# Kernel tuning notes

Measured on AMD Instinct MI355X. Metric: run time of the kernel, lower is better.

The kernel has to match this reference:

```python
import jax, jax.numpy as jnp
import numpy as np

NEG = -1.0e9

def setup_inputs() -> dict:
    key = jax.random.key(0)
    ks = jax.random.split(key, 4)
    B, S, D, DK = 4, 2048, 1024, 128
    inputs = jax.random.normal(ks[0], (B, S, D), dtype=jnp.float32)
    scale = 1.0 / np.sqrt(D)
    Wq = jax.random.normal(ks[1], (D, DK), dtype=jnp.float32) * scale
    Wk = jax.random.normal(ks[2], (D, DK), dtype=jnp.float32) * scale
    Wv = jax.random.normal(ks[3], (D, DK), dtype=jnp.float32) * scale
    bq = jnp.zeros((DK,), dtype=jnp.float32)
    bk = jnp.zeros((DK,), dtype=jnp.float32)
    bv = jnp.zeros((DK,), dtype=jnp.float32)
    return {"inputs": inputs, "Wq": Wq, "bq": bq, "Wk": Wk, "bk": bk, "Wv": Wv, "bv": bv}

def reference(inputs, Wq, bq, Wk, bk, Wv, bv):
    # Q/K/V projections: Dense(d_k) on last dim
    Q = jnp.einsum('bsd,dk->bsk', inputs, Wq) + bq
    K = jnp.einsum('bsd,dk->bsk', inputs, Wk) + bk
    V = jnp.einsum('bsd,dk->bsk', inputs, Wv) + bv
    d_k = Q.shape[-1]
    S = inputs.shape[1]
    # FAITHFUL to original bug: mask = lower-triangular ones, added *-1e9
    # (masks the lower triangle including the diagonal, NOT the upper).
    mask = jnp.tril(jnp.ones((S, S), dtype=inputs.dtype))
    scores = jnp.einsum('bqk,bsk->bqs', Q, K) / jnp.sqrt(jnp.asarray(d_k, inputs.dtype))
    masked_scores = scores + mask * NEG  # [B, S, S]
    attn = jax.nn.softmax(masked_scores, axis=-1)
    out = jnp.einsum('bqs,bsk->bqk', attn, V)  # [B, S, d_k]
    return out
```

## Files before the change

### kernel.cpp

```cpp
#include <hip/hip_runtime.h>
#include <hip/hip_bf16.h>

typedef __attribute__((ext_vector_type(8))) short bf16x8;
typedef __attribute__((ext_vector_type(4))) float f32x4;

#define QSCALE 0.088388347648318447f

__device__ __forceinline__ unsigned short f2bf(float f) {
  __hip_bfloat16 h = __float2bfloat16(f);
  unsigned short u;
  __builtin_memcpy(&u, &h, 2);
  return u;
}
__device__ __forceinline__ float bf2f(unsigned short u) {
  unsigned int x = ((unsigned int)u) << 16;
  float f; __builtin_memcpy(&f, &x, 4);
  return f;
}

__device__ __forceinline__ void gload_lds16(void* lds, const void* g) {
  __builtin_amdgcn_global_load_lds(
      (const __attribute__((address_space(1))) unsigned int*)g,
      (__attribute__((address_space(3))) unsigned int*)lds, 16, 0, 0);
}

__global__ __launch_bounds__(256) void cvt_x(const float* __restrict__ x,
                                             unsigned short* __restrict__ xb) {
  int i = (blockIdx.x * 256 + threadIdx.x) * 8;
  float4 v0 = *reinterpret_cast<const float4*>(x + i);
  float4 v1 = *reinterpret_cast<const float4*>(x + i + 4);
  ushort4 o0, o1;
  o0.x = f2bf(v0.x); o0.y = f2bf(v0.y); o0.z = f2bf(v0.z); o0.w = f2bf(v0.w);
  o1.x = f2bf(v1.x); o1.y = f2bf(v1.y); o1.z = f2bf(v1.z); o1.w = f2bf(v1.w);
  *reinterpret_cast<ushort4*>(xb + i) = o0;
  *reinterpret_cast<ushort4*>(xb + i + 4) = o1;
}

__global__ __launch_bounds__(256) void cvt_w(const float* __restrict__ Wq,
                                             const float* __restrict__ Wk,
                                             const float* __restrict__ Wv,
                                             unsigned short* __restrict__ Wt) {
  int idx = blockIdx.x * 256 + threadIdx.x;
  int n = idx >> 10, d = idx & 1023;
  const float* W = (n < 128) ? Wq : (n < 256 ? Wk : Wv);
  float v = W[d * 128 + (n & 127)];
  if (n < 128) v *= QSCALE;
  Wt[idx] = f2bf(v);
}

__global__ __launch_bounds__(256) void proj_gemm(
    const unsigned short* __restrict__ Xb, const unsigned short* __restrict__ Wt,
    const float* __restrict__ bq, const float* __restrict__ bk, const float* __restrict__ bv,
    unsigned short* __restrict__ Qb, unsigned short* __restrict__ Kb,
    unsigned short* __restrict__ Vt) {
  __shared__ unsigned short sA[64 * 64];
  __shared__ unsigned short sB[64 * 64];
  const int nt = blockIdx.x % 6;
  const int mt = blockIdx.x / 6;
  const int m0 = mt * 64;
  const int n0 = nt * 64;
  const int tid = threadIdx.x;
  const int lane = tid & 63;
  const int w = tid >> 6;
  const int r = lane & 15, g = lane >> 4;
  const int wm = (w >> 1) * 32, wn = (w & 1) * 32;

  f32x4 acc[2][2];
  #pragma unroll
  for (int mi = 0; mi < 2; ++mi)
    #pragma unroll
    for (int ni = 0; ni < 2; ++ni)
      acc[mi][ni] = (f32x4){0.f, 0.f, 0.f, 0.f};

  const char* Ab = (const char*)Xb;
  const char* Bb = (const char*)Wt;
  char* sAb = (char*)sA;
  char* sBb = (char*)sB;

  for (int k0 = 0; k0 < 1024; k0 += 64) {
    #pragma unroll
    for (int j = 0; j < 2; ++j) {
      int f = j * 4096 + tid * 16;
      int row = f >> 7;
      int colb = f & 127;
      gload_lds16(sAb + f, Ab + ((size_t)(m0 + row) * 1024 + k0) * 2 + colb);
      gload_lds16(sBb + f, Bb + ((size_t)(n0 + row) * 1024 + k0) * 2 + colb);
    }
    __syncthreads();
    #pragma unroll
    for (int kk = 0; kk < 2; ++kk) {
      bf16x8 af[2], bfr[2];
      #pragma unroll
      for (int mi = 0; mi < 2; ++mi)
        af[mi] = *reinterpret_cast<const bf16x8*>(sA + (wm + mi * 16 + r) * 64 + kk * 32 + g * 8);
      #pragma unroll
      for (int ni = 0; ni < 2; ++ni)
        bfr[ni] = *reinterpret_cast<const bf16x8*>(sB + (wn + ni * 16 + r) * 64 + kk * 32 + g * 8);
      #pragma unroll
      for (int mi = 0; mi < 2; ++mi)
        #pragma unroll
        for (int ni = 0; ni < 2; ++ni)
          acc[mi][ni] = __builtin_amdgcn_mfma_f32_16x16x32_bf16(af[mi], bfr[ni], acc[mi][ni], 0, 0, 0);
    }
    __syncthreads();
  }

  const float* bias = (nt < 2) ? bq : (nt < 4 ? bk : bv);
  const float bsc = (nt < 2) ? QSCALE : 1.0f;
  #pragma unroll
  for (int mi = 0; mi < 2; ++mi) {
    #pragma unroll
    for (int ni = 0; ni < 2; ++ni) {
      const int colg = n0 + wn + ni * 16 + r;
      const int colm = colg & 127;
      const float bias_v = bias[colm] * bsc;
      #pragma unroll
      for (int e = 0; e < 4; ++e) {
        const int row = m0 + wm + mi * 16 + g * 4 + e;
        const unsigned short hh = f2bf(acc[mi][ni][e] + bias_v);
        if (nt < 2) Qb[(size_t)row * 128 + colm] = hh;
        else if (nt < 4) Kb[(size_t)row * 128 + colm] = hh;
        else {
          const int bb = row >> 11, s = row & 2047;
          Vt[((size_t)bb * 128 + colm) * 2048 + s] = hh;
        }
      }
    }
  }
}

__global__ __launch_bounds__(512, 4) void attn(
    const unsigned short* __restrict__ Qb, const unsigned short* __restrict__ Kb,
    const unsigned short* __restrict__ Vt,
    float* __restrict__ po, float* __restrict__ pl) {
  __shared__ char sK[2][8192];
  __shared__ char sV[2][8192];
  __shared__ unsigned short pbuf_s[8][512];
  const int tid = threadIdx.x;
  const int lane = tid & 63;
  const int w = tid >> 6;
  const int r = lane & 15, g = lane >> 4;
  const int sig = blockIdx.x & 7;
  const int b = (blockIdx.x >> 3) & 3;
  const int p = blockIdx.x >> 5;

  const char* Kg = (const char*)(Kb + (size_t)b * 2048 * 128);
  const char* Vg = (const char*)(Vt + (size_t)b * 128 * 2048);
  unsigned short* pbuf = pbuf_s[w];

  const int krow = tid >> 4;
  const int kcol = ((tid & 15) * 16) ^ ((krow & 7) * 16);
  const int vrow = tid >> 2;
  const int vcol = ((tid & 3) * 16) ^ ((vrow & 3) * 16);

  for (int phase = 0; phase < 2; ++phase) {
    const int t = phase ? (15 - p) : p;
    const int q0b = t << 7;
    const int ntiles = (2048 - q0b) >> 5;
    const int q0w = q0b + w * 16;

    const unsigned short* Q = Qb + (size_t)(b * 2048 + q0w) * 128;
    bf16x8 qf[4];
    #pragma unroll
    for (int kk = 0; kk < 4; ++kk)
      qf[kk] = *reinterpret_cast<const bf16x8*>(Q + r * 128 + kk * 32 + g * 8);

    f32x4 o[8];
    #pragma unroll
    for (int ni = 0; ni < 8; ++ni) o[ni] = (f32x4){0.f, 0.f, 0.f, 0.f};
    float l[4];
    #pragma unroll
    for (int e = 0; e < 4; ++e) l[e] = 0.f;

    const int nT = (ntiles > sig) ? ((ntiles - sig + 7) >> 3) : 0;

    if (nT > 0) {
      const int s0 = q0b + (sig << 5);
      gload_lds16(&sK[0][tid * 16], Kg + (size_t)(s0 + krow) * 256 + kcol);
      gload_lds16(&sV[0][tid * 16], Vg + (size_t)vrow * 4096 + (size_t)s0 * 2 + vcol);
    }
    for (int it = 0; it < nT; ++it) {
      const int cur = it & 1;
      const int s0 = q0b + ((sig + (it << 3)) << 5);
      if (it + 1 < nT) {
        const int s1 = s0 + 256;
        gload_lds16(&sK[cur ^ 1][tid * 16], Kg + (size_t)(s1 + krow) * 256 + kcol);
        gload_lds16(&sV[cur ^ 1][tid * 16], Vg + (size_t)vrow * 4096 + (size_t)s1 * 2 + vcol);
        asm volatile("s_waitcnt vmcnt(2)" ::: "memory");
      } else {
        asm volatile("s_waitcnt vmcnt(0)" ::: "memory");
      }
      asm volatile("s_barrier" ::: "memory");

      f32x4 st[2];
      #pragma unroll
      for (int sj = 0; sj < 2; ++sj) {
        f32x4 a = (f32x4){0.f, 0.f, 0.f, 0.f};
        #pragma unroll
        for (int kk = 0; kk < 4; ++kk) {
          const bf16x8 kf = *reinterpret_cast<const bf16x8*>(
              &sK[cur][(sj * 16 + r) * 256 + (((kk * 64 + g * 16) ^ ((r & 7) * 16)))]);
          a = __builtin_amdgcn_mfma_f32_16x16x32_bf16(qf[kk], kf, a, 0, 0, 0);
        }
        st[sj] = a;
      }
      #pragma unroll
      for (int sj = 0; sj < 2; ++sj) {
        const int s = s0 + sj * 16 + r;
        #pragma unroll
        for (int e = 0; e < 4; ++e) {
          const int q = q0w + g * 4 + e;
          st[sj][e] = (s <= q) ? 0.f : __expf(st[sj][e]);
        }
      }
      #pragma unroll
      for (int e = 0; e < 4; ++e) l[e] += st[0][e] + st[1][e];

      #pragma unroll
      for (int sj = 0; sj < 2; ++sj)
        #pragma unroll
        for (int e = 0; e < 4; ++e)
          pbuf[(g * 4 + e) * 32 + sj * 16 + r] = f2bf(st[sj][e]);
      asm volatile("s_waitcnt lgkmcnt(0)" ::: "memory");
      __builtin_amdgcn_sched_barrier(0);
      const bf16x8 pa = *reinterpret_cast<const bf16x8*>(&pbuf[r * 32 + g * 8]);

      #pragma unroll
      for (int ni = 0; ni < 8; ++ni) {
        const bf16x8 vf = *reinterpret_cast<const bf16x8*>(
            &sV[cur][(ni * 16 + r) * 64 + ((g * 16) ^ ((r & 3) * 16))]);
        o[ni] = __builtin_amdgcn_mfma_f32_16x16x32_bf16(pa, vf, o[ni], 0, 0, 0);
      }
      asm volatile("s_waitcnt lgkmcnt(0)" ::: "memory");
      __builtin_amdgcn_sched_barrier(0);
      asm volatile("s_barrier" ::: "memory");
    }

    #pragma unroll
    for (int off = 1; off < 16; off <<= 1)
      #pragma unroll
      for (int e = 0; e < 4; ++e)
        l[e] += __shfl_xor(l[e], off, 64);

    const size_t pb = ((size_t)((b * 16 + t) * 8 + sig)) * 16384;
    #pragma unroll
    for (int ni = 0; ni < 8; ++ni)
      #pragma unroll
      for (int e = 0; e < 4; ++e)
        po[pb + (size_t)(w * 16 + g * 4 + e) * 128 + ni * 16 + r] = o[ni][e];
    if (r == 0) {
      #pragma unroll
      for (int e = 0; e < 4; ++e)
        pl[((size_t)((b * 16 + t) * 8 + sig)) * 128 + w * 16 + g * 4 + e] = l[e];
    }
  }
}

__global__ __launch_bounds__(256) void combine(const float* __restrict__ po,
                                               const float* __restrict__ pl,
                                               float* __restrict__ out) {
  const int idx = blockIdx.x * 256 + threadIdx.x;
  const int d = idx & 127;
  const int gq = idx >> 7;
  const int b = gq >> 11, q = gq & 2047;
  const int qt = q >> 7, row = q & 127;
  const size_t base = (size_t)(b * 16 + qt) * 8;
  float o = 0.f, l = 0.f;
  #pragma unroll
  for (int s = 0; s < 8; ++s) {
    o += po[(base + s) * 16384 + row * 128 + d];
    l += pl[(base + s) * 128 + row];
  }
  out[idx] = (l > 0.f) ? o / l : 0.f;
}

__global__ __launch_bounds__(64) void lastrow(const unsigned short* __restrict__ Vt,
                                              float* __restrict__ out) {
  const int b = blockIdx.x >> 7;
  const int dk = blockIdx.x & 127;
  const unsigned short* row = Vt + (size_t)(b * 128 + dk) * 2048;
  float s = 0.f;
  for (int i = threadIdx.x; i < 2048; i += 64) s += bf2f(row[i]);
  #pragma unroll
  for (int off = 32; off > 0; off >>= 1) s += __shfl_down(s, off, 64);
  if (threadIdx.x == 0) out[(size_t)(b * 2048 + 2047) * 128 + dk] = s * (1.0f / 2048.0f);
}

extern "C" void kernel_launch(void* const* d_in, const int* in_sizes, int n_in,
                              void* d_out, int out_size, void* d_ws, size_t ws_size,
                              hipStream_t stream) {
  const float* x  = (const float*)d_in[0];
  const float* Wq = (const float*)d_in[1];
  const float* bq = (const float*)d_in[2];
  const float* Wk = (const float*)d_in[3];
  const float* bk = (const float*)d_in[4];
  const float* Wv = (const float*)d_in[5];
  const float* bv = (const float*)d_in[6];
  float* out = (float*)d_out;
  char* ws = (char*)d_ws;
  unsigned short* Xb = (unsigned short*)(ws);
  unsigned short* Wt = (unsigned short*)(ws + (size_t)(16u << 20));
  unsigned short* Qb = (unsigned short*)(ws + (size_t)(17u << 20));
  unsigned short* Kb = (unsigned short*)(ws + (size_t)(19u << 20));
  unsigned short* Vt = (unsigned short*)(ws + (size_t)(21u << 20));
  float* po = (float*)(ws + (size_t)(24u << 20));
  float* pl = (float*)(ws + (size_t)(56u << 20));

  hipLaunchKernelGGL(cvt_x, dim3(4096), dim3(256), 0, stream, x, Xb);
  hipLaunchKernelGGL(cvt_w, dim3(1536), dim3(256), 0, stream, Wq, Wk, Wv, Wt);
  hipLaunchKernelGGL(proj_gemm, dim3(768), dim3(256), 0, stream,
                     Xb, Wt, bq, bk, bv, Qb, Kb, Vt);
  hipLaunchKernelGGL(attn, dim3(256), dim3(512), 0, stream, Qb, Kb, Vt, po, pl);
  hipLaunchKernelGGL(combine, dim3(4096), dim3(256), 0, stream, po, pl, out);
  hipLaunchKernelGGL(lastrow, dim3(512), dim3(64), 0, stream, Vt, out);
}
```

Baseline: 71.83 us.

## Merge conversion kernels and enlarge projection GEMM tiles to 128x96

Merges the input and weight bf16 conversion kernels into one launch, removing a kernel launch and its gap. Reworks the projection GEMM to use 512-thread blocks computing 128x96 output tiles instead of 64x64, so 256 blocks cover the full 8192x384 output. Bias and destination selection now happen per column because a tile can straddle the Q, K and V boundaries. Larger tiles reuse each loaded operand for more MFMAs, but the grid is only 256 blocks, roughly one per CU, so there is less latency hiding.

```diff
diff --git a/kernel.cpp b/kernel.cpp
--- a/kernel.cpp
+++ b/kernel.cpp
@@ -24,52 +24,54 @@
       (__attribute__((address_space(3))) unsigned int*)lds, 16, 0, 0);
 }
 
-__global__ __launch_bounds__(256) void cvt_x(const float* __restrict__ x,
-                                             unsigned short* __restrict__ xb) {
-  int i = (blockIdx.x * 256 + threadIdx.x) * 8;
-  float4 v0 = *reinterpret_cast<const float4*>(x + i);
-  float4 v1 = *reinterpret_cast<const float4*>(x + i + 4);
-  ushort4 o0, o1;
-  o0.x = f2bf(v0.x); o0.y = f2bf(v0.y); o0.z = f2bf(v0.z); o0.w = f2bf(v0.w);
-  o1.x = f2bf(v1.x); o1.y = f2bf(v1.y); o1.z = f2bf(v1.z); o1.w = f2bf(v1.w);
-  *reinterpret_cast<ushort4*>(xb + i) = o0;
-  *reinterpret_cast<ushort4*>(xb + i + 4) = o1;
-}
-
-__global__ __launch_bounds__(256) void cvt_w(const float* __restrict__ Wq,
-                                             const float* __restrict__ Wk,
-                                             const float* __restrict__ Wv,
-                                             unsigned short* __restrict__ Wt) {
-  int idx = blockIdx.x * 256 + threadIdx.x;
-  int n = idx >> 10, d = idx & 1023;
-  const float* W = (n < 128) ? Wq : (n < 256 ? Wk : Wv);
-  float v = W[d * 128 + (n & 127)];
-  if (n < 128) v *= QSCALE;
-  Wt[idx] = f2bf(v);
-}
-
-__global__ __launch_bounds__(256) void proj_gemm(
+__global__ __launch_bounds__(256) void cvt(const float* __restrict__ x,
+                                           unsigned short* __restrict__ xb,
+                                           const float* __restrict__ Wq,
+                                           const float* __restrict__ Wk,
+                                           const float* __restrict__ Wv,
+                                           unsigned short* __restrict__ Wt) {
+  const int bid = blockIdx.x;
+  if (bid < 4096) {
+    int i = (bid * 256 + threadIdx.x) * 8;
+    float4 v0 = *reinterpret_cast<const float4*>(x + i);
+    float4 v1 = *reinterpret_cast<const float4*>(x + i + 4);
+    ushort4 o0, o1;
+    o0.x = f2bf(v0.x); o0.y = f2bf(v0.y); o0.z = f2bf(v0.z); o0.w = f2bf(v0.w);
+    o1.x = f2bf(v1.x); o1.y = f2bf(v1.y); o1.z = f2bf(v1.z); o1.w = f2bf(v1.w);
+    *reinterpret_cast<ushort4*>(xb + i) = o0;
+    *reinterpret_cast<ushort4*>(xb + i + 4) = o1;
+  } else {
+    int idx = (bid - 4096) * 256 + threadIdx.x;
+    int n = idx >> 10, d = idx & 1023;
+    const float* W = (n < 128) ? Wq : (n < 256 ? Wk : Wv);
+    float v = W[d * 128 + (n & 127)];
+    if (n < 128) v *= QSCALE;
+    Wt[idx] = f2bf(v);
+  }
+}
+
+__global__ __launch_bounds__(512) void proj_gemm(
     const unsigned short* __restrict__ Xb, const unsigned short* __restrict__ Wt,
     const float* __restrict__ bq, const float* __restrict__ bk, const float* __restrict__ bv,
     unsigned short* __restrict__ Qb, unsigned short* __restrict__ Kb,
     unsigned short* __restrict__ Vt) {
-  __shared__ unsigned short sA[64 * 64];
-  __shared__ unsigned short sB[64 * 64];
-  const int nt = blockIdx.x % 6;
-  const int mt = blockIdx.x / 6;
-  const int m0 = mt * 64;
-  const int n0 = nt * 64;
+  __shared__ unsigned short sA[128 * 64];
+  __shared__ unsigned short sB[96 * 64];
+  const int nt = blockIdx.x & 3;
+  const int mt = blockIdx.x >> 2;
+  const int m0 = mt * 128;
+  const int n0 = nt * 96;
   const int tid = threadIdx.x;
   const int lane = tid & 63;
   const int w = tid >> 6;
   const int r = lane & 15, g = lane >> 4;
-  const int wm = (w >> 1) * 32, wn = (w & 1) * 32;
-
-  f32x4 acc[2][2];
+  const int wm = (w >> 1) * 32, wn = (w & 1) * 48;
+
+  f32x4 acc[2][3];
   #pragma unroll
   for (int mi = 0; mi < 2; ++mi)
     #pragma unroll
-    for (int ni = 0; ni < 2; ++ni)
+    for (int ni = 0; ni < 3; ++ni)
       acc[mi][ni] = (f32x4){0.f, 0.f, 0.f, 0.f};
 
   const char* Ab = (const char*)Xb;
@@ -80,46 +82,54 @@
   for (int k0 = 0; k0 < 1024; k0 += 64) {
     #pragma unroll
     for (int j = 0; j < 2; ++j) {
-      int f = j * 4096 + tid * 16;
-      int row = f >> 7;
-      int colb = f & 127;
+      int f = j * 8192 + tid * 16;
+      int row = f >> 7, colb = f & 127;
       gload_lds16(sAb + f, Ab + ((size_t)(m0 + row) * 1024 + k0) * 2 + colb);
+    }
+    {
+      int f = tid * 16;
+      int row = f >> 7, colb = f & 127;
       gload_lds16(sBb + f, Bb + ((size_t)(n0 + row) * 1024 + k0) * 2 + colb);
+      if (tid < 256) {
+        int f2 = 8192 + tid * 16;
+        int row2 = f2 >> 7, colb2 = f2 & 127;
+        gload_lds16(sBb + f2, Bb + ((size_t)(n0 + row2) * 1024 + k0) * 2 + colb2);
+      }
     }
     __syncthreads();
     #pragma unroll
     for (int kk = 0; kk < 2; ++kk) {
-      bf16x8 af[2], bfr[2];
+      bf16x8 af[2], bfr[3];
       #pragma unroll
       for (int mi = 0; mi < 2; ++mi)
         af[mi] = *reinterpret_cast<const bf16x8*>(sA + (wm + mi * 16 + r) * 64 + kk * 32 + g * 8);
       #pragma unroll
-      for (int ni = 0; ni < 2; ++ni)
+      for (int ni = 0; ni < 3; ++ni)
         bfr[ni] = *reinterpret_cast<const bf16x8*>(sB + (wn + ni * 16 + r) * 64 + kk * 32 + g * 8);
       #pragma unroll
       for (int mi = 0; mi < 2; ++mi)
         #pragma unroll
-        for (int ni = 0; ni < 2; ++ni)
+        for (int ni = 0; ni < 3; ++ni)
           acc[mi][ni] = __builtin_amdgcn_mfma_f32_16x16x32_bf16(af[mi], bfr[ni], acc[mi][ni], 0, 0, 0);
     }
     __syncthreads();
   }
 
-  const float* bias = (nt < 2) ? bq : (nt < 4 ? bk : bv);
-  const float bsc = (nt < 2) ? QSCALE : 1.0f;
   #pragma unroll
   for (int mi = 0; mi < 2; ++mi) {
     #pragma unroll
-    for (int ni = 0; ni < 2; ++ni) {
+    for (int ni = 0; ni < 3; ++ni) {
       const int colg = n0 + wn + ni * 16 + r;
+      const int which = colg >> 7;
       const int colm = colg & 127;
-      const float bias_v = bias[colm] * bsc;
+      const float* bias = (which == 0) ? bq : (which == 1 ? bk : bv);
+      const float bias_v = bias[colm] * ((which == 0) ? QSCALE : 1.0f);
       #pragma unroll
       for (int e = 0; e < 4; ++e) {
         const int row = m0 + wm + mi * 16 + g * 4 + e;
         const unsigned short hh = f2bf(acc[mi][ni][e] + bias_v);
-        if (nt < 2) Qb[(size_t)row * 128 + colm] = hh;
-        else if (nt < 4) Kb[(size_t)row * 128 + colm] = hh;
+        if (which == 0) Qb[(size_t)row * 128 + colm] = hh;
+        else if (which == 1) Kb[(size_t)row * 128 + colm] = hh;
         else {
           const int bb = row >> 11, s = row & 2047;
           Vt[((size_t)bb * 128 + colm) * 2048 + s] = hh;
@@ -306,9 +316,8 @@
   float* po = (float*)(ws + (size_t)(24u << 20));
   float* pl = (float*)(ws + (size_t)(56u << 20));
 
-  hipLaunchKernelGGL(cvt_x, dim3(4096), dim3(256), 0, stream, x, Xb);
-  hipLaunchKernelGGL(cvt_w, dim3(1536), dim3(256), 0, stream, Wq, Wk, Wv, Wt);
-  hipLaunchKernelGGL(proj_gemm, dim3(768), dim3(256), 0, stream,
+  hipLaunchKernelGGL(cvt, dim3(5632), dim3(256), 0, stream, x, Xb, Wq, Wk, Wv, Wt);
+  hipLaunchKernelGGL(proj_gemm, dim3(256), dim3(512), 0, stream,
                      Xb, Wt, bq, bk, bv, Qb, Kb, Vt);
   hipLaunchKernelGGL(attn, dim3(256), dim3(512), 0, stream, Qb, Kb, Vt, po, pl);
   hipLaunchKernelGGL(combine, dim3(4096), dim3(256), 0, stream, po, pl, out);
```

New measurement: 77.79 us. 1.08x slower.
